# Optimization experiments

Hardware: AMD Instinct MI355X
Metric: run time of the kernel (lower is better)

Reference implementation:

```python
import jax, jax.numpy as jnp
import numpy as np

N_NODES = 50000
F_IN = 256
HEADS = 8
C = 256 // HEADS  # out channels per head (output_dim // heads)
NEG_SLOPE = 0.2


def setup_inputs() -> dict:
    key = jax.random.key(0)
    k_x, k_e, k_w, k_as, k_ad, k_b = jax.random.split(key, 6)
    x = jax.random.normal(k_x, (N_NODES, F_IN), dtype=jnp.float32)
    edge_index = jax.random.randint(k_e, (2, 800000), 0, N_NODES, dtype=jnp.int32)
    # GATConv params: linear weight, per-head attention vectors, bias
    s = 1.0 / np.sqrt(F_IN)
    W = jax.random.uniform(k_w, (F_IN, HEADS * C), jnp.float32, -s, s)
    att_src = jax.random.uniform(k_as, (HEADS, C), jnp.float32, -s, s)
    att_dst = jax.random.uniform(k_ad, (HEADS, C), jnp.float32, -s, s)
    bias = jnp.zeros((HEADS * C,), jnp.float32)
    return {"x": x, "edge_index": edge_index, "W": W,
            "att_src": att_src, "att_dst": att_dst, "bias": bias}


def _gat_forward(x, edge_index, W, att_src, att_dst, bias):
    N = x.shape[0]
    # add self loops (PyG GATConv default add_self_loops=True)
    loops = jnp.arange(N, dtype=edge_index.dtype)
    src = jnp.concatenate([edge_index[0], loops])
    dst = jnp.concatenate([edge_index[1], loops])

    h = (x @ W).reshape(N, HEADS, C)                       # [N,H,C]
    a_src = jnp.einsum('nhc,hc->nh', h, att_src)           # [N,H]
    a_dst = jnp.einsum('nhc,hc->nh', h, att_dst)           # [N,H]

    alpha = a_src[src] + a_dst[dst]                        # [E2,H]
    alpha = jax.nn.leaky_relu(alpha, NEG_SLOPE)
    # softmax over incoming edges of each dst node, per head
    amax = jax.ops.segment_max(alpha, dst, num_segments=N)
    amax = jnp.where(jnp.isfinite(amax), amax, 0.0)
    ex = jnp.exp(alpha - amax[dst])
    denom = jax.ops.segment_sum(ex, dst, num_segments=N) + 1e-16
    attn = ex / denom[dst]                                 # [E2,H]

    msg = h[src] * attn[:, :, None]                        # [E2,H,C]
    out = jax.ops.segment_sum(msg, dst, num_segments=N)    # [N,H,C]
    out = out.reshape(N, HEADS * C) + bias
    return jax.nn.elu(out)


def reference(x, edge_index, W, att_src, att_dst, bias):
    return _gat_forward(x, edge_index, W, att_src, att_dst, bias)
```

## Files before the change

### kernel.cpp

```cpp
#include <hip/hip_runtime.h>
#include <hip/hip_bf16.h>
#include <math.h>

#define F_IN 256
#define HEADS 8
#define CPH 32
#define NEG_SLOPE 0.2f

typedef short bf16x8 __attribute__((ext_vector_type(8)));
typedef float f32x4  __attribute__((ext_vector_type(4)));
typedef _Float16 half4 __attribute__((ext_vector_type(4)));

static __device__ __forceinline__ unsigned short f2bf(float f) {
    union { float f; unsigned int u; } v; v.f = f;
    unsigned int r = (v.u + 0x7FFFu + ((v.u >> 16) & 1u)) >> 16;
    return (unsigned short)r;
}
static __device__ __forceinline__ float bf2f(unsigned short h) {
    union { unsigned int u; float f; } v; v.u = ((unsigned int)h) << 16;
    return v.f;
}

__global__ __launch_bounds__(256) void wprep_kernel(
    const float* __restrict__ W, short* __restrict__ WtHi, short* __restrict__ WtLo)
{
    const int k = blockIdx.x;
    const int n = threadIdx.x;
    const float w = W[(size_t)k * 256 + n];
    const unsigned short h = f2bf(w);
    const unsigned short l = f2bf(w - bf2f(h));
    const int step = k >> 5, kg = (k >> 3) & 3, j = k & 7;
    const size_t dst = ((((size_t)step * 4 + kg) * 256) + n) * 8 + j;
    WtHi[dst] = (short)h;
    WtLo[dst] = (short)l;
}

__global__ __launch_bounds__(256, 2) void gemm_mfma_kernel(
    const float* __restrict__ X, const short* __restrict__ WtHi,
    const short* __restrict__ WtLo, _Float16* __restrict__ H2, int M)
{
    __shared__ short Ah[4][128][8];
    __shared__ short Al[4][128][8];
    __shared__ short Bh[4][128][8];
    __shared__ short Bl[4][128][8];

    const int t    = threadIdx.x;
    const int lane = t & 63;
    const int wid  = t >> 6;
    const int wr   = wid >> 1;
    const int wc   = wid & 1;
    const int row0 = blockIdx.x * 128;
    const int col0 = blockIdx.y * 128;

    const int srow  = t >> 1;
    const int shalf = t & 1;

    f32x4 acc[4][4];
#pragma unroll
    for (int i = 0; i < 4; ++i)
#pragma unroll
        for (int j = 0; j < 4; ++j)
            acc[i][j] = (f32x4){0.f, 0.f, 0.f, 0.f};

    const int kgf = lane >> 4;
    const int lrow = lane & 15;

    for (int step = 0; step < 8; ++step) {
        const int k0 = step * 32;
        float f[16];
        const int grow = row0 + srow;
        if (grow < M) {
            const float4* xp = (const float4*)(X + (size_t)grow * 256 + k0 + shalf * 16);
            const float4 v0 = xp[0], v1 = xp[1], v2 = xp[2], v3 = xp[3];
            f[0] = v0.x; f[1] = v0.y; f[2]  = v0.z; f[3]  = v0.w;
            f[4] = v1.x; f[5] = v1.y; f[6]  = v1.z; f[7]  = v1.w;
            f[8] = v2.x; f[9] = v2.y; f[10] = v2.z; f[11] = v2.w;
            f[12] = v3.x; f[13] = v3.y; f[14] = v3.z; f[15] = v3.w;
        } else {
#pragma unroll
            for (int j = 0; j < 16; ++j) f[j] = 0.f;
        }
#pragma unroll
        for (int c = 0; c < 2; ++c) {
            bf16x8 hi, lo;
#pragma unroll
            for (int j = 0; j < 8; ++j) {
                const float x = f[c * 8 + j];
                const unsigned short hb = f2bf(x);
                hi[j] = (short)hb;
                lo[j] = (short)f2bf(x - bf2f(hb));
            }
            const int kg = shalf * 2 + c;
            *(bf16x8*)&Ah[kg][srow][0] = hi;
            *(bf16x8*)&Al[kg][srow][0] = lo;
        }
#pragma unroll
        for (int rep = 0; rep < 2; ++rep) {
            const int s  = t + rep * 256;
            const int kg = s >> 7;
            const int nl = s & 127;
            const size_t src = ((((size_t)step * 4 + kg) * 256) + col0 + nl) * 8;
            *(bf16x8*)&Bh[kg][nl][0] = *(const bf16x8*)&WtHi[src];
            *(bf16x8*)&Bl[kg][nl][0] = *(const bf16x8*)&WtLo[src];
        }
        __syncthreads();

        bf16x8 ah[4], al[4];
#pragma unroll
        for (int i = 0; i < 4; ++i) {
            const int rl = wr * 64 + i * 16 + lrow;
            ah[i] = *(const bf16x8*)&Ah[kgf][rl][0];
            al[i] = *(const bf16x8*)&Al[kgf][rl][0];
        }
#pragma unroll
        for (int j = 0; j < 4; ++j) {
            const int cl = wc * 64 + j * 16 + lrow;
            const bf16x8 bh = *(const bf16x8*)&Bh[kgf][cl][0];
            const bf16x8 bl = *(const bf16x8*)&Bl[kgf][cl][0];
#pragma unroll
            for (int i = 0; i < 4; ++i) {
                acc[i][j] = __builtin_amdgcn_mfma_f32_16x16x32_bf16(al[i], bh, acc[i][j], 0, 0, 0);
                acc[i][j] = __builtin_amdgcn_mfma_f32_16x16x32_bf16(ah[i], bl, acc[i][j], 0, 0, 0);
                acc[i][j] = __builtin_amdgcn_mfma_f32_16x16x32_bf16(ah[i], bh, acc[i][j], 0, 0, 0);
            }
        }
        __syncthreads();
    }

    const int cbase = col0 + wc * 64 + lrow;
    const int rbase = row0 + wr * 64 + (lane >> 4) * 4;
#pragma unroll
    for (int i = 0; i < 4; ++i) {
#pragma unroll
        for (int r = 0; r < 4; ++r) {
            const int row = rbase + i * 16 + r;
            if (row < M) {
#pragma unroll
                for (int j = 0; j < 4; ++j)
                    H2[(size_t)row * 256 + cbase + j * 16] = (_Float16)acc[i][j][r];
            }
        }
    }
}

__global__ __launch_bounds__(256) void attdot_kernel(
    const _Float16* __restrict__ H2, const float* __restrict__ att_src,
    const float* __restrict__ att_dst, float* __restrict__ a_src,
    float* __restrict__ a_dst, int N)
{
    const int n = (int)((blockIdx.x * blockDim.x + threadIdx.x) >> 6);
    const int lane = threadIdx.x & 63;
    if (n >= N) return;
    const half4 hv = *(const half4*)(H2 + (size_t)n * 256 + lane * 4);
    const float4 as = *(const float4*)(att_src + lane * 4);
    const float4 ad = *(const float4*)(att_dst + lane * 4);
    const float h0 = (float)hv[0], h1 = (float)hv[1], h2 = (float)hv[2], h3 = (float)hv[3];
    float s = h0 * as.x + h1 * as.y + h2 * as.z + h3 * as.w;
    float d = h0 * ad.x + h1 * ad.y + h2 * ad.z + h3 * ad.w;
#pragma unroll
    for (int off = 1; off < 8; off <<= 1) {
        s += __shfl_xor(s, off);
        d += __shfl_xor(d, off);
    }
    if ((lane & 7) == 0) {
        a_src[(size_t)n * 8 + (lane >> 3)] = s;
        a_dst[(size_t)n * 8 + (lane >> 3)] = d;
    }
}

__global__ __launch_bounds__(256) void hist_kernel(
    const int* __restrict__ ei, int* __restrict__ deg, int E, int E2)
{
    const int e = blockIdx.x * blockDim.x + threadIdx.x;
    if (e >= E2) return;
    const int dst = (e < E) ? ei[(size_t)E + e] : (e - E);
    atomicAdd(&deg[dst], 1);
}

__global__ __launch_bounds__(256) void scan_reduce_kernel(
    const int* __restrict__ deg, int* __restrict__ partial, int n)
{
    const int i = blockIdx.x * 256 + threadIdx.x;
    int v = (i < n) ? deg[i] : 0;
#pragma unroll
    for (int off = 1; off < 64; off <<= 1) v += __shfl_xor(v, off);
    __shared__ int s[4];
    if ((threadIdx.x & 63) == 0) s[threadIdx.x >> 6] = v;
    __syncthreads();
    if (threadIdx.x == 0) partial[blockIdx.x] = s[0] + s[1] + s[2] + s[3];
}

__global__ __launch_bounds__(256) void scan_partials_kernel(
    int* __restrict__ partial, int nb)
{
    __shared__ int tmp[256];
    const int t = threadIdx.x;
    const int v = (t < nb) ? partial[t] : 0;
    tmp[t] = v;
    __syncthreads();
    for (int off = 1; off < 256; off <<= 1) {
        int add = (t >= off) ? tmp[t - off] : 0;
        __syncthreads();
        tmp[t] += add;
        __syncthreads();
    }
    if (t < nb) partial[t] = tmp[t] - v;
}

__global__ __launch_bounds__(256) void scan_final_kernel(
    const int* __restrict__ deg, const int* __restrict__ partial,
    int* __restrict__ offsets, int n, int total)
{
    __shared__ int tmp[256];
    const int t = threadIdx.x;
    const int i = blockIdx.x * 256 + t;
    const int v = (i < n) ? deg[i] : 0;
    tmp[t] = v;
    __syncthreads();
    for (int off = 1; off < 256; off <<= 1) {
        int add = (t >= off) ? tmp[t - off] : 0;
        __syncthreads();
        tmp[t] += add;
        __syncthreads();
    }
    if (i < n) offsets[i] = partial[blockIdx.x] + tmp[t] - v;
    if (i == 0) offsets[n] = total;
}

__global__ __launch_bounds__(256) void scatter_kernel(
    const int* __restrict__ ei, const int* __restrict__ offsets,
    int* __restrict__ cursor, int* __restrict__ sorted_src, int E, int E2)
{
    const int e = blockIdx.x * blockDim.x + threadIdx.x;
    if (e >= E2) return;
    int src, dst;
    if (e < E) { src = ei[e]; dst = ei[(size_t)E + e]; }
    else       { src = e - E; dst = e - E; }
    const int pos = atomicAdd(&cursor[dst], 1);
    sorted_src[offsets[dst] + pos] = src;
}

__global__ __launch_bounds__(256) void aggregate_kernel(
    const _Float16* __restrict__ H2, const float* __restrict__ Asrc,
    const float* __restrict__ Adst, const int* __restrict__ offsets,
    const int* __restrict__ sorted_src, const float* __restrict__ bias,
    float* __restrict__ out, int N)
{
    const int n = (int)((blockIdx.x * blockDim.x + threadIdx.x) >> 6);
    const int lane = threadIdx.x & 63;
    if (n >= N) return;

    const int beg = offsets[n];
    const int deg = offsets[n + 1] - beg;

    const int h2 = lane & 7;
    const float adst2 = Adst[(size_t)n * 8 + h2];

    float m = -INFINITY;
    float ssum = 0.f;
    for (int i = lane; i < deg * 8; i += 64) {
        const int s = sorted_src[beg + (i >> 3)];
        float a = Asrc[(size_t)s * 8 + h2] + adst2;
        a = a > 0.f ? a : NEG_SLOPE * a;
        if (a > m) { ssum *= expf(m - a); m = a; }
        ssum += expf(a - m);
    }
#pragma unroll
    for (int off = 8; off < 64; off <<= 1) {
        const float mo = __shfl_xor(m, off);
        const float so = __shfl_xor(ssum, off);
        const float mn = fmaxf(m, mo);
        const float f1 = (m  <= -INFINITY) ? 0.f : expf(m  - mn);
        const float f2 = (mo <= -INFINITY) ? 0.f : expf(mo - mn);
        ssum = ssum * f1 + so * f2;
        m = mn;
    }

    const int h3 = lane >> 3;
    const float m3 = __shfl(m, h3);
    const float d3 = __shfl(ssum, h3);
    const float adst3 = __shfl(adst2, h3);
    const float rdn = 1.f / (d3 + 1e-16f);

    float4 acc0 = make_float4(0.f, 0.f, 0.f, 0.f);
    float4 acc1 = make_float4(0.f, 0.f, 0.f, 0.f);
    int e = 0;
    for (; e + 4 <= deg; e += 4) {
        const int s0 = sorted_src[beg + e];
        const int s1 = sorted_src[beg + e + 1];
        const int s2 = sorted_src[beg + e + 2];
        const int s3 = sorted_src[beg + e + 3];
        const half4 g0 = *(const half4*)(H2 + (size_t)s0 * 256 + lane * 4);
        const half4 g1 = *(const half4*)(H2 + (size_t)s1 * 256 + lane * 4);
        const half4 g2 = *(const half4*)(H2 + (size_t)s2 * 256 + lane * 4);
        const half4 g3 = *(const half4*)(H2 + (size_t)s3 * 256 + lane * 4);
        float a0 = Asrc[(size_t)s0 * 8 + h3] + adst3;
        float a1 = Asrc[(size_t)s1 * 8 + h3] + adst3;
        float a2 = Asrc[(size_t)s2 * 8 + h3] + adst3;
        float a3 = Asrc[(size_t)s3 * 8 + h3] + adst3;
        a0 = a0 > 0.f ? a0 : NEG_SLOPE * a0;
        a1 = a1 > 0.f ? a1 : NEG_SLOPE * a1;
        a2 = a2 > 0.f ? a2 : NEG_SLOPE * a2;
        a3 = a3 > 0.f ? a3 : NEG_SLOPE * a3;
        const float w0 = expf(a0 - m3) * rdn;
        const float w1 = expf(a1 - m3) * rdn;
        const float w2 = expf(a2 - m3) * rdn;
        const float w3 = expf(a3 - m3) * rdn;
        acc0.x += (float)g0[0] * w0; acc0.y += (float)g0[1] * w0; acc0.z += (float)g0[2] * w0; acc0.w += (float)g0[3] * w0;
        acc1.x += (float)g1[0] * w1; acc1.y += (float)g1[1] * w1; acc1.z += (float)g1[2] * w1; acc1.w += (float)g1[3] * w1;
        acc0.x += (float)g2[0] * w2; acc0.y += (float)g2[1] * w2; acc0.z += (float)g2[2] * w2; acc0.w += (float)g2[3] * w2;
        acc1.x += (float)g3[0] * w3; acc1.y += (float)g3[1] * w3; acc1.z += (float)g3[2] * w3; acc1.w += (float)g3[3] * w3;
    }
    for (; e < deg; ++e) {
        const int s0 = sorted_src[beg + e];
        const half4 g0 = *(const half4*)(H2 + (size_t)s0 * 256 + lane * 4);
        float a0 = Asrc[(size_t)s0 * 8 + h3] + adst3;
        a0 = a0 > 0.f ? a0 : NEG_SLOPE * a0;
        const float w0 = expf(a0 - m3) * rdn;
        acc0.x += (float)g0[0] * w0; acc0.y += (float)g0[1] * w0; acc0.z += (float)g0[2] * w0; acc0.w += (float)g0[3] * w0;
    }
    float4 acc;
    acc.x = acc0.x + acc1.x; acc.y = acc0.y + acc1.y;
    acc.z = acc0.z + acc1.z; acc.w = acc0.w + acc1.w;

    const float4 b = *(const float4*)(bias + lane * 4);
    float4 o;
    o.x = acc.x + b.x; o.y = acc.y + b.y; o.z = acc.z + b.z; o.w = acc.w + b.w;
    o.x = o.x > 0.f ? o.x : expf(o.x) - 1.f;
    o.y = o.y > 0.f ? o.y : expf(o.y) - 1.f;
    o.z = o.z > 0.f ? o.z : expf(o.z) - 1.f;
    o.w = o.w > 0.f ? o.w : expf(o.w) - 1.f;
    *(float4*)(out + (size_t)n * 256 + lane * 4) = o;
}

extern "C" void kernel_launch(void* const* d_in, const int* in_sizes, int n_in,
                              void* d_out, int out_size, void* d_ws, size_t ws_size,
                              hipStream_t stream)
{
    const float* x       = (const float*)d_in[0];
    const int*   ei      = (const int*)  d_in[1];
    const float* W       = (const float*)d_in[2];
    const float* att_src = (const float*)d_in[3];
    const float* att_dst = (const float*)d_in[4];
    const float* bias    = (const float*)d_in[5];
    float* out = (float*)d_out;

    const int N  = in_sizes[0] / F_IN;
    const int E  = in_sizes[1] / 2;
    const int E2 = E + N;
    const int NB = (N + 255) / 256;

    char* ws = (char*)d_ws;
    size_t o = 0;
    auto take = [&](size_t bytes) { void* p = ws + o; o = (o + bytes + 255) & ~(size_t)255; return p; };
    _Float16* H2      = (_Float16*)take((size_t)N * 256 * 2);
    float* a_src      = (float*)take((size_t)N * 8 * 4);
    float* a_dst      = (float*)take((size_t)N * 8 * 4);
    int*   deg        = (int*)  take((size_t)N * 4 * 2);
    int*   cursor     = deg + N;
    int*   offsets    = (int*)  take((size_t)(N + 1) * 4);
    int*   sorted_src = (int*)  take((size_t)E2 * 4);
    int*   partial    = (int*)  take((size_t)NB * 4);
    short* WtHi       = (short*)take((size_t)256 * 256 * 2);
    short* WtLo       = (short*)take((size_t)256 * 256 * 2);
    (void)ws_size; (void)n_in; (void)out_size;

    hipMemsetAsync(deg, 0, (size_t)N * 4 * 2, stream);

    wprep_kernel<<<256, 256, 0, stream>>>(W, WtHi, WtLo);
    dim3 ggrid((N + 127) / 128, 2);
    gemm_mfma_kernel<<<ggrid, 256, 0, stream>>>(x, WtHi, WtLo, H2, N);

    attdot_kernel<<<(N * 64 + 255) / 256, 256, 0, stream>>>(H2, att_src, att_dst, a_src, a_dst, N);

    hist_kernel<<<(E2 + 255) / 256, 256, 0, stream>>>(ei, deg, E, E2);
    scan_reduce_kernel<<<NB, 256, 0, stream>>>(deg, partial, N);
    scan_partials_kernel<<<1, 256, 0, stream>>>(partial, NB);
    scan_final_kernel<<<NB, 256, 0, stream>>>(deg, partial, offsets, N, E2);
    scatter_kernel<<<(E2 + 255) / 256, 256, 0, stream>>>(ei, offsets, cursor, sorted_src, E, E2);

    aggregate_kernel<<<(N * 64 + 255) / 256, 256, 0, stream>>>(H2, a_src, a_dst, offsets, sorted_src, bias, out, N);
}
```

Before: 308.8 us.

## Cache per-edge attention logits and source ids in LDS for aggregation

The aggregate kernel now computes leaky-relu logits once per edge and stores them, along with source indices, in per-wave shared memory (up to 128 edges). It then does a two-pass max/sum softmax and pre-normalizes the weights in place. The gather loop reads weights and ids from LDS instead of recomputing exp and re-reading Asrc and sorted_src from global memory. It also switches to fast __expf, which loses some accuracy, and adds LDS use that may lower occupancy.

Result: faster. 300.3 us (-2.8%).

```diff
diff --git a/kernel.cpp b/kernel.cpp
--- a/kernel.cpp
+++ b/kernel.cpp
@@ -6,6 +6,7 @@
 #define HEADS 8
 #define CPH 32
 #define NEG_SLOPE 0.2f
+#define MAXD 128
 
 typedef short bf16x8 __attribute__((ext_vector_type(8)));
 typedef float f32x4  __attribute__((ext_vector_type(4)));
@@ -19,6 +20,11 @@
 static __device__ __forceinline__ float bf2f(unsigned short h) {
     union { unsigned int u; float f; } v; v.u = ((unsigned int)h) << 16;
     return v.f;
+}
+
+static __device__ __forceinline__ void lds_fence() {
+    asm volatile("s_waitcnt lgkmcnt(0)" ::: "memory");
+    __builtin_amdgcn_sched_barrier(0);
 }
 
 __global__ __launch_bounds__(256) void wprep_kernel(
@@ -246,77 +252,96 @@
     const int* __restrict__ sorted_src, const float* __restrict__ bias,
     float* __restrict__ out, int N)
 {
+    __shared__ float aw[4][MAXD][8];
+    __shared__ int   sid[4][MAXD];
+
     const int n = (int)((blockIdx.x * blockDim.x + threadIdx.x) >> 6);
     const int lane = threadIdx.x & 63;
+    const int wid  = (threadIdx.x >> 6) & 3;
     if (n >= N) return;
 
     const int beg = offsets[n];
     const int deg = offsets[n + 1] - beg;
+    const int dcap = deg < MAXD ? deg : MAXD;
 
     const int h2 = lane & 7;
     const float adst2 = Adst[(size_t)n * 8 + h2];
 
     float m = -INFINITY;
+    for (int i = lane; i < deg * 8; i += 64) {
+        const int e = i >> 3;
+        const int s = sorted_src[beg + e];
+        float a = Asrc[(size_t)s * 8 + h2] + adst2;
+        a = a > 0.f ? a : NEG_SLOPE * a;
+        if (e < MAXD) {
+            aw[wid][e][h2] = a;
+            if (h2 == 0) sid[wid][e] = s;
+        }
+        m = fmaxf(m, a);
+    }
+#pragma unroll
+    for (int off = 8; off < 64; off <<= 1) m = fmaxf(m, __shfl_xor(m, off));
+    lds_fence();
+
     float ssum = 0.f;
     for (int i = lane; i < deg * 8; i += 64) {
-        const int s = sorted_src[beg + (i >> 3)];
-        float a = Asrc[(size_t)s * 8 + h2] + adst2;
-        a = a > 0.f ? a : NEG_SLOPE * a;
-        if (a > m) { ssum *= expf(m - a); m = a; }
-        ssum += expf(a - m);
-    }
-#pragma unroll
-    for (int off = 8; off < 64; off <<= 1) {
-        const float mo = __shfl_xor(m, off);
-        const float so = __shfl_xor(ssum, off);
-        const float mn = fmaxf(m, mo);
-        const float f1 = (m  <= -INFINITY) ? 0.f : expf(m  - mn);
-        const float f2 = (mo <= -INFINITY) ? 0.f : expf(mo - mn);
-        ssum = ssum * f1 + so * f2;
-        m = mn;
-    }
+        const int e = i >> 3;
+        float a;
+        if (e < MAXD) {
+            a = aw[wid][e][h2];
+        } else {
+            const int s = sorted_src[beg + e];
+            a = Asrc[(size_t)s * 8 + h2] + adst2;
+            a = a > 0.f ? a : NEG_SLOPE * a;
+        }
+        const float w = __expf(a - m);
+        ssum += w;
+        if (e < MAXD) aw[wid][e][h2] = w;
+    }
+#pragma unroll
+    for (int off = 8; off < 64; off <<= 1) ssum += __shfl_xor(ssum, off);
+    const float rdn = 1.f / (ssum + 1e-16f);
+    lds_fence();
+
+    for (int i = lane; i < dcap * 8; i += 64)
+        aw[wid][i >> 3][h2] *= rdn;
+    lds_fence();
 
     const int h3 = lane >> 3;
-    const float m3 = __shfl(m, h3);
-    const float d3 = __shfl(ssum, h3);
+    const float m3   = __shfl(m, h3);
+    const float rdn3 = __shfl(rdn, h3);
     const float adst3 = __shfl(adst2, h3);
-    const float rdn = 1.f / (d3 + 1e-16f);
 
     float4 acc0 = make_float4(0.f, 0.f, 0.f, 0.f);
     float4 acc1 = make_float4(0.f, 0.f, 0.f, 0.f);
     int e = 0;
-    for (; e + 4 <= deg; e += 4) {
-        const int s0 = sorted_src[beg + e];
-        const int s1 = sorted_src[beg + e + 1];
-        const int s2 = sorted_src[beg + e + 2];
-        const int s3 = sorted_src[beg + e + 3];
-        const half4 g0 = *(const half4*)(H2 + (size_t)s0 * 256 + lane * 4);
-        const half4 g1 = *(const half4*)(H2 + (size_t)s1 * 256 + lane * 4);
-        const half4 g2 = *(const half4*)(H2 + (size_t)s2 * 256 + lane * 4);
-        const half4 g3 = *(const half4*)(H2 + (size_t)s3 * 256 + lane * 4);
-        float a0 = Asrc[(size_t)s0 * 8 + h3] + adst3;
-        float a1 = Asrc[(size_t)s1 * 8 + h3] + adst3;
-        float a2 = Asrc[(size_t)s2 * 8 + h3] + adst3;
-        float a3 = Asrc[(size_t)s3 * 8 + h3] + adst3;
-        a0 = a0 > 0.f ? a0 : NEG_SLOPE * a0;
-        a1 = a1 > 0.f ? a1 : NEG_SLOPE * a1;
-        a2 = a2 > 0.f ? a2 : NEG_SLOPE * a2;
-        a3 = a3 > 0.f ? a3 : NEG_SLOPE * a3;
-        const float w0 = expf(a0 - m3) * rdn;
-        const float w1 = expf(a1 - m3) * rdn;
-        const float w2 = expf(a2 - m3) * rdn;
-        const float w3 = expf(a3 - m3) * rdn;
+    for (; e + 4 <= dcap; e += 4) {
+        const int4 s4 = *(const int4*)&sid[wid][e];
+        const float w0 = aw[wid][e + 0][h3];
+        const float w1 = aw[wid][e + 1][h3];
+        const float w2 = aw[wid][e + 2][h3];
+        const float w3 = aw[wid][e + 3][h3];
+        const half4 g0 = *(const half4*)(H2 + (size_t)s4.x * 256 + lane * 4);
+        const half4 g1 = *(const half4*)(H2 + (size_t)s4.y * 256 + lane * 4);
+        const half4 g2 = *(const half4*)(H2 + (size_t)s4.z * 256 + lane * 4);
+        const half4 g3 = *(const half4*)(H2 + (size_t)s4.w * 256 + lane * 4);
         acc0.x += (float)g0[0] * w0; acc0.y += (float)g0[1] * w0; acc0.z += (float)g0[2] * w0; acc0.w += (float)g0[3] * w0;
         acc1.x += (float)g1[0] * w1; acc1.y += (float)g1[1] * w1; acc1.z += (float)g1[2] * w1; acc1.w += (float)g1[3] * w1;
         acc0.x += (float)g2[0] * w2; acc0.y += (float)g2[1] * w2; acc0.z += (float)g2[2] * w2; acc0.w += (float)g2[3] * w2;
         acc1.x += (float)g3[0] * w3; acc1.y += (float)g3[1] * w3; acc1.z += (float)g3[2] * w3; acc1.w += (float)g3[3] * w3;
     }
+    for (; e < dcap; ++e) {
+        const int s0 = sid[wid][e];
+        const float w0 = aw[wid][e][h3];
+        const half4 g0 = *(const half4*)(H2 + (size_t)s0 * 256 + lane * 4);
+        acc0.x += (float)g0[0] * w0; acc0.y += (float)g0[1] * w0; acc0.z += (float)g0[2] * w0; acc0.w += (float)g0[3] * w0;
+    }
     for (; e < deg; ++e) {
         const int s0 = sorted_src[beg + e];
-        const half4 g0 = *(const half4*)(H2 + (size_t)s0 * 256 + lane * 4);
         float a0 = Asrc[(size_t)s0 * 8 + h3] + adst3;
         a0 = a0 > 0.f ? a0 : NEG_SLOPE * a0;
-        const float w0 = expf(a0 - m3) * rdn;
+        const float w0 = __expf(a0 - m3) * rdn3;
+        const half4 g0 = *(const half4*)(H2 + (size_t)s0 * 256 + lane * 4);
         acc0.x += (float)g0[0] * w0; acc0.y += (float)g0[1] * w0; acc0.z += (float)g0[2] * w0; acc0.w += (float)g0[3] * w0;
     }
     float4 acc;
@@ -326,10 +351,10 @@
     const float4 b = *(const float4*)(bias + lane * 4);
     float4 o;
     o.x = acc.x + b.x; o.y = acc.y + b.y; o.z = acc.z + b.z; o.w = acc.w + b.w;
-    o.x = o.x > 0.f ? o.x : expf(o.x) - 1.f;
-    o.y = o.y > 0.f ? o.y : expf(o.y) - 1.f;
-    o.z = o.z > 0.f ? o.z : expf(o.z) - 1.f;
-    o.w = o.w > 0.f ? o.w : expf(o.w) - 1.f;
+    o.x = o.x > 0.f ? o.x : __expf(o.x) - 1.f;
+    o.y = o.y > 0.f ? o.y : __expf(o.y) - 1.f;
+    o.z = o.z > 0.f ? o.z : __expf(o.z) - 1.f;
+    o.w = o.w > 0.f ? o.w : __expf(o.w) - 1.f;
     *(float4*)(out + (size_t)n * 256 + lane * 4) = o;
 }
 
```
